# Kernel tuning notes

Hardware: AMD Instinct MI355X
Metric: run time of the kernel (lower is better)

The kernel has to match this reference:

```python
import jax, jax.numpy as jnp
import numpy as np

T, K = 2048, 6          # tokens, activated experts per token
DIM = 2048              # model dim
INTER = 1408            # moe intermediate dim
E = 16                  # routed experts (group_size, shared not fused)


def setup_inputs() -> dict:
    key = jax.random.key(0)
    k1, k2, k3, k4, k5, k6 = jax.random.split(key, 6)
    x = jax.random.normal(k1, (T, DIM), dtype=jnp.float32)
    weights = jax.random.uniform(k2, (T, K), dtype=jnp.float32)
    indices = jax.random.randint(k3, (T, K), 0, E, dtype=jnp.int64)
    s = 1.0 / np.sqrt(DIM)
    Wg = jax.random.normal(k4, (E, INTER, DIM), dtype=jnp.float32) * s
    Wu = jax.random.normal(k5, (E, INTER, DIM), dtype=jnp.float32) * s
    Wd = jax.random.normal(k6, (E, DIM, INTER), dtype=jnp.float32) * (1.0 / np.sqrt(INTER))
    return {"x": x, "weights": weights, "indices": indices,
            "Wg": Wg, "Wu": Wu, "Wd": Wd}


def reference(x, weights, indices, Wg, Wu, Wd):
    # per-token combine weight for each expert: [T, E]
    # gate_w[t, e] = sum_k weights[t, k] * (indices[t, k] == e)
    one_hot = jax.nn.one_hot(indices, E, dtype=x.dtype)        # [T, K, E]
    gate_w = jnp.einsum('tk,tke->te', weights, one_hot)        # [T, E]

    # SwiGLU expert FFN, dense over experts, combine folded pre-down-proj
    g = jnp.einsum('td,eid->tei', x, Wg)                       # [T, E, INTER]
    u = jnp.einsum('td,eid->tei', x, Wu)                       # [T, E, INTER]
    act = jax.nn.silu(g) * u                                   # [T, E, INTER]
    # y[t] = sum_e gate_w[t,e] * (act[t,e] @ Wd[e].T)
    y = jnp.einsum('tei,edi->td', act * gate_w[:, :, None], Wd)  # [T, DIM]
    return y
```

## Files before the change

### kernel.cpp

```cpp
#include <hip/hip_runtime.h>
#include <hip/hip_bf16.h>
#include <cstdint>

#define TT     2048
#define KSEL   6
#define DMODEL 2048
#define DINTER 1408
#define NE     16
#define PMAX   (TT * KSEL)

typedef short bf16x8 __attribute__((ext_vector_type(8)));
typedef float f32x4 __attribute__((ext_vector_type(4)));
typedef unsigned short u16;
typedef u16 u16x8 __attribute__((ext_vector_type(8)));

__device__ __forceinline__ u16 f2bf(float f) {
  union { float f; unsigned u; } v; v.f = f;
  return (u16)((v.u + 0x7FFFu + ((v.u >> 16) & 1u)) >> 16);
}

__device__ __forceinline__ void gl2lds16(const void* g, void* l) {
  __builtin_amdgcn_global_load_lds((const __attribute__((address_space(1))) void*)g,
                                   (__attribute__((address_space(3))) void*)l,
                                   16, 0, 0);
}

__global__ void k_gate(const float* __restrict__ w, const int* __restrict__ idx,
                       float* __restrict__ gate_w, int* __restrict__ counts) {
  int g = blockIdx.x * 256 + threadIdx.x;
  int t = g >> 4, e = g & 15;
  const int* ip = idx + t * KSEL;
  const float* wp = w + t * KSEL;
  float s = 0.f;
#pragma unroll
  for (int k = 0; k < KSEL; ++k) s += (ip[k] == e) ? wp[k] : 0.f;
  gate_w[g] = s;
  if (s != 0.f) atomicAdd(counts + e, 1);
}

__global__ void k_scan(const int* __restrict__ counts, int* __restrict__ offs) {
  if (threadIdx.x == 0 && blockIdx.x == 0) {
    int r = 0;
#pragma unroll
    for (int e = 0; e < NE; ++e) { offs[e] = r; r += counts[e]; }
    offs[NE] = r;
  }
}

__global__ void k_fill(const float* __restrict__ gate_w, const int* __restrict__ offs,
                       int* __restrict__ cursor, int* __restrict__ slot_tok,
                       float* __restrict__ slot_gate) {
  int g = blockIdx.x * 256 + threadIdx.x;
  int t = g >> 4, e = g & 15;
  float s = gate_w[g];
  if (s != 0.f) {
    int p = atomicAdd(cursor + e, 1);
    int sl = offs[e] + p;
    slot_tok[sl] = t;
    slot_gate[sl] = s;
  }
}

#define XV8   (TT * DMODEL / 8)
#define WV8   (NE * DINTER * DMODEL / 8)
__global__ void k_castall(const float* __restrict__ x,  u16* __restrict__ xb,
                          const float* __restrict__ wg, u16* __restrict__ wgb,
                          const float* __restrict__ wu, u16* __restrict__ wub,
                          const float* __restrict__ wd, u16* __restrict__ wdb) {
  const int total = XV8 + 3 * WV8;
  int stride = gridDim.x * 256;
  for (int i = blockIdx.x * 256 + threadIdx.x; i < total; i += stride) {
    const float* src; u16* dst; int j;
    if (i < XV8)                { src = x;  dst = xb;  j = i; }
    else if (i < XV8 + WV8)     { src = wg; dst = wgb; j = i - XV8; }
    else if (i < XV8 + 2 * WV8) { src = wu; dst = wub; j = i - XV8 - WV8; }
    else                        { src = wd; dst = wdb; j = i - XV8 - 2 * WV8; }
    const float4* p = (const float4*)src + (size_t)j * 2;
    float4 v0 = p[0], v1 = p[1];
    u16x8 o;
    o[0] = f2bf(v0.x); o[1] = f2bf(v0.y); o[2] = f2bf(v0.z); o[3] = f2bf(v0.w);
    o[4] = f2bf(v1.x); o[5] = f2bf(v1.y); o[6] = f2bf(v1.z); o[7] = f2bf(v1.w);
    *(u16x8*)(dst + (size_t)j * 8) = o;
  }
}


__global__ __launch_bounds__(256, 2) void k_gemm1(
    const u16* __restrict__ xb, const u16* __restrict__ wgb, const u16* __restrict__ wub,
    const int* __restrict__ slot_tok, const float* __restrict__ slot_gate,
    const int* __restrict__ offs, const int* __restrict__ counts,
    u16* __restrict__ act) {
  int b = blockIdx.x;
  int w = (b & 7) * 352 + (b >> 3);
  int mt = w & 15, rest = w >> 4;
  int it = rest % 11, e = rest / 11;

  int mcount = counts[e];
  if (mt * 128 >= mcount) return;
  int mrem = mcount - mt * 128; if (mrem > 128) mrem = 128;
  int slotBase = offs[e] + mt * 128;
  int iBase = it * 128;

  __shared__ u16 sA[128 * 64];
  __shared__ u16 sG[128 * 64];
  __shared__ u16 sU[128 * 64];
  __shared__ int tokLds[128];
  __shared__ float gateLds[128];

  int tid = threadIdx.x;
  if (tid < 128) {
    int rl = tid < mrem ? tid : 0;
    tokLds[tid] = slot_tok[slotBase + rl];
    gateLds[tid] = (tid < mrem) ? slot_gate[slotBase + rl] : 0.f;
  }
  __syncthreads();

  int wv = tid >> 6, lane = tid & 63;
  const u16 *aSrc[4], *gSrc[4], *uSrc[4];
  u16 *aDst[4], *gDst[4], *uDst[4];
  const u16* gBase = wgb + ((size_t)e * DINTER + iBase) * DMODEL;
  const u16* uBase = wub + ((size_t)e * DINTER + iBase) * DMODEL;
  int r8 = lane >> 3;
  int colOff = ((lane & 7) ^ r8) * 8;
#pragma unroll
  for (int i2 = 0; i2 < 4; ++i2) {
    int chunk = wv * 4 + i2;
    int row = chunk * 8 + r8;
    aSrc[i2] = xb + (size_t)tokLds[row] * DMODEL + colOff;
    gSrc[i2] = gBase + (size_t)row * DMODEL + colOff;
    uSrc[i2] = uBase + (size_t)row * DMODEL + colOff;
    aDst[i2] = sA + chunk * 512;
    gDst[i2] = sG + chunk * 512;
    uDst[i2] = sU + chunk * 512;
  }

  f32x4 accg[4][4] = {};
  f32x4 accu[4][4] = {};
  int fr = lane & 15, fq = lane >> 4;
  int wr = (wv >> 1) * 64, wc = (wv & 1) * 64;

  for (int kb = 0; kb < DMODEL / 64; ++kb) {
    int kOff = kb * 64;
    __syncthreads();
#pragma unroll
    for (int i2 = 0; i2 < 4; ++i2) {
      gl2lds16(aSrc[i2] + kOff, aDst[i2]);
      gl2lds16(gSrc[i2] + kOff, gDst[i2]);
      gl2lds16(uSrc[i2] + kOff, uDst[i2]);
    }
    __syncthreads();
#pragma unroll
    for (int kf = 0; kf < 2; ++kf) {
      bf16x8 af[4], bg[4], bu[4];
#pragma unroll
      for (int mf = 0; mf < 4; ++mf) {
        int row = wr + mf * 16 + fr;
        int cu = ((kf * 4 + fq) ^ (row & 7)) * 8;
        af[mf] = *(const bf16x8*)&sA[row * 64 + cu];
      }
#pragma unroll
      for (int nf = 0; nf < 4; ++nf) {
        int row = wc + nf * 16 + fr;
        int cu = ((kf * 4 + fq) ^ (row & 7)) * 8;
        bg[nf] = *(const bf16x8*)&sG[row * 64 + cu];
        bu[nf] = *(const bf16x8*)&sU[row * 64 + cu];
      }
#pragma unroll
      for (int mf = 0; mf < 4; ++mf)
#pragma unroll
        for (int nf = 0; nf < 4; ++nf) {
          accg[mf][nf] = __builtin_amdgcn_mfma_f32_16x16x32_bf16(af[mf], bg[nf], accg[mf][nf], 0, 0, 0);
          accu[mf][nf] = __builtin_amdgcn_mfma_f32_16x16x32_bf16(af[mf], bu[nf], accu[mf][nf], 0, 0, 0);
        }
    }
  }
#pragma unroll
  for (int mf = 0; mf < 4; ++mf)
#pragma unroll
    for (int nf = 0; nf < 4; ++nf)
#pragma unroll
      for (int r = 0; r < 4; ++r) {
        int row = wr + mf * 16 + fq * 4 + r;
        if (row < mrem) {
          float g = accg[mf][nf][r], u = accu[mf][nf][r];
          float a = g / (1.f + __expf(-g)) * u * gateLds[row];
          act[(size_t)(slotBase + row) * DINTER + iBase + wc + nf * 16 + fr] = f2bf(a);
        }
      }
}

__global__ __launch_bounds__(256, 3) void k_gemm2(
    const u16* __restrict__ act, const u16* __restrict__ wdb,
    const int* __restrict__ slot_tok, const int* __restrict__ offs,
    const int* __restrict__ counts, float* __restrict__ y) {
  int b = blockIdx.x;
  int w = (b & 7) * 512 + (b >> 3);
  int mt = w & 15, rest = w >> 4;
  int dt = rest & 15, e = rest >> 4;

  int mcount = counts[e];
  if (mt * 128 >= mcount) return;
  int mrem = mcount - mt * 128; if (mrem > 128) mrem = 128;
  int slotBase = offs[e] + mt * 128;
  int dBase = dt * 128;

  __shared__ u16 sA[128 * 64];
  __shared__ u16 sB[128 * 64];
  __shared__ int tokLds[128];

  int tid = threadIdx.x;
  if (tid < 128) tokLds[tid] = slot_tok[slotBase + (tid < mrem ? tid : 0)];
  __syncthreads();

  int wv = tid >> 6, lane = tid & 63;
  const u16 *aSrc[4], *bSrc[4];
  u16 *aDst[4], *bDst[4];
  const u16* bBase = wdb + ((size_t)e * DMODEL + dBase) * DINTER;
  int r8 = lane >> 3;
  int colOff = ((lane & 7) ^ r8) * 8;
#pragma unroll
  for (int i2 = 0; i2 < 4; ++i2) {
    int chunk = wv * 4 + i2;
    int row = chunk * 8 + r8;
    aSrc[i2] = act + (size_t)(slotBase + row) * DINTER + colOff;
    bSrc[i2] = bBase + (size_t)row * DINTER + colOff;
    aDst[i2] = sA + chunk * 512;
    bDst[i2] = sB + chunk * 512;
  }

  f32x4 acc[4][4] = {};
  int fr = lane & 15, fq = lane >> 4;
  int wr = (wv >> 1) * 64, wc = (wv & 1) * 64;

  for (int kb = 0; kb < DINTER / 64; ++kb) {
    int kOff = kb * 64;
    __syncthreads();
#pragma unroll
    for (int i2 = 0; i2 < 4; ++i2) {
      gl2lds16(aSrc[i2] + kOff, aDst[i2]);
      gl2lds16(bSrc[i2] + kOff, bDst[i2]);
    }
    __syncthreads();
#pragma unroll
    for (int kf = 0; kf < 2; ++kf) {
      bf16x8 af[4], bb[4];
#pragma unroll
      for (int mf = 0; mf < 4; ++mf) {
        int row = wr + mf * 16 + fr;
        int cu = ((kf * 4 + fq) ^ (row & 7)) * 8;
        af[mf] = *(const bf16x8*)&sA[row * 64 + cu];
      }
#pragma unroll
      for (int nf = 0; nf < 4; ++nf) {
        int row = wc + nf * 16 + fr;
        int cu = ((kf * 4 + fq) ^ (row & 7)) * 8;
        bb[nf] = *(const bf16x8*)&sB[row * 64 + cu];
      }
#pragma unroll
      for (int mf = 0; mf < 4; ++mf)
#pragma unroll
        for (int nf = 0; nf < 4; ++nf)
          acc[mf][nf] = __builtin_amdgcn_mfma_f32_16x16x32_bf16(af[mf], bb[nf], acc[mf][nf], 0, 0, 0);
    }
  }
#pragma unroll
  for (int mf = 0; mf < 4; ++mf)
#pragma unroll
    for (int nf = 0; nf < 4; ++nf)
#pragma unroll
      for (int r = 0; r < 4; ++r) {
        int row = wr + mf * 16 + fq * 4 + r;
        if (row < mrem) {
          int t = tokLds[row];
          atomicAdd(y + (size_t)t * DMODEL + dBase + wc + nf * 16 + fr, acc[mf][nf][r]);
        }
      }
}

extern "C" void kernel_launch(void* const* d_in, const int* in_sizes, int n_in,
                              void* d_out, int out_size, void* d_ws, size_t ws_size,
                              hipStream_t stream) {
  const float* x       = (const float*)d_in[0];
  const float* weights = (const float*)d_in[1];
  const int*   indices = (const int*)d_in[2];
  const float* Wg      = (const float*)d_in[3];
  const float* Wu      = (const float*)d_in[4];
  const float* Wd      = (const float*)d_in[5];
  float* y = (float*)d_out;

  const size_t WELEM = (size_t)NE * DINTER * DMODEL;

  char* ws = (char*)d_ws;
  size_t o = 0;
  float* gate_w = (float*)(ws + o); o += (size_t)TT * NE * 4;
  size_t ctrlOff = o;
  int* counts = (int*)(ws + o);
  int* offs   = (int*)(ws + o + 64);
  int* cursor = (int*)(ws + o + 192);
  o += 256;
  int*   slot_tok  = (int*)(ws + o);   o += (size_t)PMAX * 4;
  float* slot_gate = (float*)(ws + o); o += (size_t)PMAX * 4;
  u16* xb  = (u16*)(ws + o); o += (size_t)TT * DMODEL * 2;
  u16* act = (u16*)(ws + o); o += (size_t)(PMAX + 128) * DINTER * 2;
  u16* wgb = (u16*)(ws + o); o += WELEM * 2;
  u16* wub = (u16*)(ws + o); o += WELEM * 2;
  u16* wdb = (u16*)(ws + o); o += WELEM * 2;
  (void)ws_size; (void)in_sizes; (void)n_in;

  hipMemsetAsync(d_out, 0, (size_t)out_size * 4, stream);
  hipMemsetAsync(ws + ctrlOff, 0, 256, stream);

  k_gate<<<TT * NE / 256, 256, 0, stream>>>(weights, indices, gate_w, counts);
  k_scan<<<1, 64, 0, stream>>>(counts, offs);
  k_fill<<<TT * NE / 256, 256, 0, stream>>>(gate_w, offs, cursor, slot_tok, slot_gate);
  k_castall<<<2048, 256, 0, stream>>>(x, xb, Wg, wgb, Wu, wub, Wd, wdb);
  k_gemm1<<<2816, 256, 0, stream>>>(xb, wgb, wub, slot_tok, slot_gate, offs, counts, act);
  k_gemm2<<<4096, 256, 0, stream>>>(act, wdb, slot_tok, offs, counts, y);
}
```

Measured before the change: 590.4 us.

## Enlarge down-projection tile to 256 rows to reuse Wd tile twice

```diff
diff --git a/kernel.cpp b/kernel.cpp
--- a/kernel.cpp
+++ b/kernel.cpp
@@ -189,32 +189,38 @@
       }
 }
 
-__global__ __launch_bounds__(256, 3) void k_gemm2(
+__global__ __launch_bounds__(256, 2) void k_gemm2(
     const u16* __restrict__ act, const u16* __restrict__ wdb,
     const int* __restrict__ slot_tok, const int* __restrict__ offs,
     const int* __restrict__ counts, float* __restrict__ y) {
   int b = blockIdx.x;
-  int w = (b & 7) * 512 + (b >> 3);
-  int mt = w & 15, rest = w >> 4;
+  int w = (b & 7) * 256 + (b >> 3);
+  int mtp = w & 7, rest = w >> 3;
   int dt = rest & 15, e = rest >> 4;
 
   int mcount = counts[e];
-  if (mt * 128 >= mcount) return;
-  int mrem = mcount - mt * 128; if (mrem > 128) mrem = 128;
-  int slotBase = offs[e] + mt * 128;
+  if (mtp * 256 >= mcount) return;
+  int rem = mcount - mtp * 256;
+  int mrem0 = rem > 128 ? 128 : rem;
+  int mrem1 = rem > 128 ? (rem - 128 > 128 ? 128 : rem - 128) : 0;
+  int slotBase = offs[e] + mtp * 256;
   int dBase = dt * 128;
 
-  __shared__ u16 sA[128 * 64];
+  __shared__ u16 sA0[128 * 64];
+  __shared__ u16 sA1[128 * 64];
   __shared__ u16 sB[128 * 64];
-  __shared__ int tokLds[128];
+  __shared__ int tokLds[256];
 
   int tid = threadIdx.x;
-  if (tid < 128) tokLds[tid] = slot_tok[slotBase + (tid < mrem ? tid : 0)];
+  if (tid < 256) {
+    int lim = rem > 256 ? 256 : rem;
+    tokLds[tid] = slot_tok[slotBase + (tid < lim ? tid : 0)];
+  }
   __syncthreads();
 
   int wv = tid >> 6, lane = tid & 63;
-  const u16 *aSrc[4], *bSrc[4];
-  u16 *aDst[4], *bDst[4];
+  const u16 *a0Src[4], *a1Src[4], *bSrc[4];
+  u16 *a0Dst[4], *a1Dst[4], *bDst[4];
   const u16* bBase = wdb + ((size_t)e * DMODEL + dBase) * DINTER;
   int r8 = lane >> 3;
   int colOff = ((lane & 7) ^ r8) * 8;
@@ -222,13 +228,16 @@
   for (int i2 = 0; i2 < 4; ++i2) {
     int chunk = wv * 4 + i2;
     int row = chunk * 8 + r8;
-    aSrc[i2] = act + (size_t)(slotBase + row) * DINTER + colOff;
-    bSrc[i2] = bBase + (size_t)row * DINTER + colOff;
-    aDst[i2] = sA + chunk * 512;
-    bDst[i2] = sB + chunk * 512;
-  }
-
-  f32x4 acc[4][4] = {};
+    a0Src[i2] = act + (size_t)(slotBase + row) * DINTER + colOff;
+    a1Src[i2] = act + (size_t)(slotBase + 128 + row) * DINTER + colOff;
+    bSrc[i2]  = bBase + (size_t)row * DINTER + colOff;
+    a0Dst[i2] = sA0 + chunk * 512;
+    a1Dst[i2] = sA1 + chunk * 512;
+    bDst[i2]  = sB + chunk * 512;
+  }
+
+  f32x4 acc0[4][4] = {};
+  f32x4 acc1[4][4] = {};
   int fr = lane & 15, fq = lane >> 4;
   int wr = (wv >> 1) * 64, wc = (wv & 1) * 64;
 
@@ -237,18 +246,20 @@
     __syncthreads();
 #pragma unroll
     for (int i2 = 0; i2 < 4; ++i2) {
-      gl2lds16(aSrc[i2] + kOff, aDst[i2]);
+      gl2lds16(a0Src[i2] + kOff, a0Dst[i2]);
+      gl2lds16(a1Src[i2] + kOff, a1Dst[i2]);
       gl2lds16(bSrc[i2] + kOff, bDst[i2]);
     }
     __syncthreads();
 #pragma unroll
     for (int kf = 0; kf < 2; ++kf) {
-      bf16x8 af[4], bb[4];
+      bf16x8 a0f[4], a1f[4], bb[4];
 #pragma unroll
       for (int mf = 0; mf < 4; ++mf) {
         int row = wr + mf * 16 + fr;
         int cu = ((kf * 4 + fq) ^ (row & 7)) * 8;
-        af[mf] = *(const bf16x8*)&sA[row * 64 + cu];
+        a0f[mf] = *(const bf16x8*)&sA0[row * 64 + cu];
+        a1f[mf] = *(const bf16x8*)&sA1[row * 64 + cu];
       }
 #pragma unroll
       for (int nf = 0; nf < 4; ++nf) {
@@ -259,8 +270,10 @@
 #pragma unroll
       for (int mf = 0; mf < 4; ++mf)
 #pragma unroll
-        for (int nf = 0; nf < 4; ++nf)
-          acc[mf][nf] = __builtin_amdgcn_mfma_f32_16x16x32_bf16(af[mf], bb[nf], acc[mf][nf], 0, 0, 0);
+        for (int nf = 0; nf < 4; ++nf) {
+          acc0[mf][nf] = __builtin_amdgcn_mfma_f32_16x16x32_bf16(a0f[mf], bb[nf], acc0[mf][nf], 0, 0, 0);
+          acc1[mf][nf] = __builtin_amdgcn_mfma_f32_16x16x32_bf16(a1f[mf], bb[nf], acc1[mf][nf], 0, 0, 0);
+        }
     }
   }
 #pragma unroll
@@ -270,9 +283,12 @@
 #pragma unroll
       for (int r = 0; r < 4; ++r) {
         int row = wr + mf * 16 + fq * 4 + r;
-        if (row < mrem) {
-          int t = tokLds[row];
-          atomicAdd(y + (size_t)t * DMODEL + dBase + wc + nf * 16 + fr, acc[mf][nf][r]);
+        int col = dBase + wc + nf * 16 + fr;
+        if (row < mrem0) {
+          atomicAdd(y + (size_t)tokLds[row] * DMODEL + col, acc0[mf][nf][r]);
+        }
+        if (row < mrem1) {
+          atomicAdd(y + (size_t)tokLds[128 + row] * DMODEL + col, acc1[mf][nf][r]);
         }
       }
 }
@@ -301,7 +317,7 @@
   int*   slot_tok  = (int*)(ws + o);   o += (size_t)PMAX * 4;
   float* slot_gate = (float*)(ws + o); o += (size_t)PMAX * 4;
   u16* xb  = (u16*)(ws + o); o += (size_t)TT * DMODEL * 2;
-  u16* act = (u16*)(ws + o); o += (size_t)(PMAX + 128) * DINTER * 2;
+  u16* act = (u16*)(ws + o); o += (size_t)(PMAX + 256) * DINTER * 2;
   u16* wgb = (u16*)(ws + o); o += WELEM * 2;
   u16* wub = (u16*)(ws + o); o += WELEM * 2;
   u16* wdb = (u16*)(ws + o); o += WELEM * 2;
@@ -315,5 +331,5 @@
   k_fill<<<TT * NE / 256, 256, 0, stream>>>(gate_w, offs, cursor, slot_tok, slot_gate);
   k_castall<<<2048, 256, 0, stream>>>(x, xb, Wg, wgb, Wu, wub, Wd, wdb);
   k_gemm1<<<2816, 256, 0, stream>>>(xb, wgb, wub, slot_tok, slot_gate, offs, counts, act);
-  k_gemm2<<<4096, 256, 0, stream>>>(act, wdb, slot_tok, offs, counts, y);
-}
+  k_gemm2<<<2048, 256, 0, stream>>>(act, wdb, slot_tok, offs, counts, y);
+}
```

Measured after the change: 601.8 us. Within noise of the previous version (+1.9%).

## Replace down-proj atomic scatter with per-slot bf16 outputs and a gather-combine kernel

Applied to the files above, without the earlier changes.

```diff
diff --git a/kernel.cpp b/kernel.cpp
--- a/kernel.cpp
+++ b/kernel.cpp
@@ -17,6 +17,9 @@
 __device__ __forceinline__ u16 f2bf(float f) {
   union { float f; unsigned u; } v; v.f = f;
   return (u16)((v.u + 0x7FFFu + ((v.u >> 16) & 1u)) >> 16);
+}
+__device__ __forceinline__ float bf2f(u16 h) {
+  union { unsigned u; float f; } v; v.u = (unsigned)h << 16; return v.f;
 }
 
 __device__ __forceinline__ void gl2lds16(const void* g, void* l) {
@@ -49,7 +52,8 @@
 
 __global__ void k_fill(const float* __restrict__ gate_w, const int* __restrict__ offs,
                        int* __restrict__ cursor, int* __restrict__ slot_tok,
-                       float* __restrict__ slot_gate) {
+                       float* __restrict__ slot_gate, int* __restrict__ tcnt,
+                       int* __restrict__ tok_slots) {
   int g = blockIdx.x * 256 + threadIdx.x;
   int t = g >> 4, e = g & 15;
   float s = gate_w[g];
@@ -58,6 +62,8 @@
     int sl = offs[e] + p;
     slot_tok[sl] = t;
     slot_gate[sl] = s;
+    int q = atomicAdd(tcnt + t, 1);
+    tok_slots[t * KSEL + q] = sl;
   }
 }
 
@@ -192,7 +198,8 @@
 __global__ __launch_bounds__(256, 3) void k_gemm2(
     const u16* __restrict__ act, const u16* __restrict__ wdb,
     const int* __restrict__ slot_tok, const int* __restrict__ offs,
-    const int* __restrict__ counts, float* __restrict__ y) {
+    const int* __restrict__ counts, float* __restrict__ y,
+    u16* __restrict__ outb) {
   int b = blockIdx.x;
   int w = (b & 7) * 512 + (b >> 3);
   int mt = w & 15, rest = w >> 4;
@@ -271,10 +278,32 @@
       for (int r = 0; r < 4; ++r) {
         int row = wr + mf * 16 + fq * 4 + r;
         if (row < mrem) {
-          int t = tokLds[row];
-          atomicAdd(y + (size_t)t * DMODEL + dBase + wc + nf * 16 + fr, acc[mf][nf][r]);
+          int col = dBase + wc + nf * 16 + fr;
+          if (outb) {
+            outb[(size_t)(slotBase + row) * DMODEL + col] = f2bf(acc[mf][nf][r]);
+          } else {
+            atomicAdd(y + (size_t)tokLds[row] * DMODEL + col, acc[mf][nf][r]);
+          }
         }
       }
+}
+
+__global__ void k_combine(const u16* __restrict__ outb, const int* __restrict__ tok_slots,
+                          const int* __restrict__ tcnt, float* __restrict__ y) {
+  int idx = blockIdx.x * 256 + threadIdx.x;
+  int t = idx >> 8;
+  int d0 = (idx & 255) * 8;
+  int n = tcnt[t];
+  float s[8] = {};
+  for (int j = 0; j < n; ++j) {
+    int sl = tok_slots[t * KSEL + j];
+    u16x8 v = *(const u16x8*)(outb + (size_t)sl * DMODEL + d0);
+#pragma unroll
+    for (int q = 0; q < 8; ++q) s[q] += bf2f(v[q]);
+  }
+  float4* yp = (float4*)(y + (size_t)t * DMODEL + d0);
+  yp[0] = make_float4(s[0], s[1], s[2], s[3]);
+  yp[1] = make_float4(s[4], s[5], s[6], s[7]);
 }
 
 extern "C" void kernel_launch(void* const* d_in, const int* in_sizes, int n_in,
@@ -297,7 +326,10 @@
   int* counts = (int*)(ws + o);
   int* offs   = (int*)(ws + o + 64);
   int* cursor = (int*)(ws + o + 192);
-  o += 256;
+  int* tcnt   = (int*)(ws + o + 256);
+  int* tok_slots = (int*)(ws + o + 256 + TT * 4);
+  size_t ctrlZero = 256 + TT * 4;
+  o += 256 + TT * 4 + (size_t)TT * KSEL * 4;
   int*   slot_tok  = (int*)(ws + o);   o += (size_t)PMAX * 4;
   float* slot_gate = (float*)(ws + o); o += (size_t)PMAX * 4;
   u16* xb  = (u16*)(ws + o); o += (size_t)TT * DMODEL * 2;
@@ -305,15 +337,23 @@
   u16* wgb = (u16*)(ws + o); o += WELEM * 2;
   u16* wub = (u16*)(ws + o); o += WELEM * 2;
   u16* wdb = (u16*)(ws + o); o += WELEM * 2;
-  (void)ws_size; (void)in_sizes; (void)n_in;
+  u16* outb = (u16*)(ws + o);
+  size_t oEnd = o + (size_t)PMAX * DMODEL * 2;
+  bool useCombine = (ws_size >= oEnd);
+  (void)in_sizes; (void)n_in;
 
   hipMemsetAsync(d_out, 0, (size_t)out_size * 4, stream);
-  hipMemsetAsync(ws + ctrlOff, 0, 256, stream);
+  hipMemsetAsync(ws + ctrlOff, 0, ctrlZero, stream);
 
   k_gate<<<TT * NE / 256, 256, 0, stream>>>(weights, indices, gate_w, counts);
   k_scan<<<1, 64, 0, stream>>>(counts, offs);
-  k_fill<<<TT * NE / 256, 256, 0, stream>>>(gate_w, offs, cursor, slot_tok, slot_gate);
+  k_fill<<<TT * NE / 256, 256, 0, stream>>>(gate_w, offs, cursor, slot_tok, slot_gate,
+                                            tcnt, tok_slots);
   k_castall<<<2048, 256, 0, stream>>>(x, xb, Wg, wgb, Wu, wub, Wd, wdb);
   k_gemm1<<<2816, 256, 0, stream>>>(xb, wgb, wub, slot_tok, slot_gate, offs, counts, act);
-  k_gemm2<<<4096, 256, 0, stream>>>(act, wdb, slot_tok, offs, counts, y);
-}
+  k_gemm2<<<4096, 256, 0, stream>>>(act, wdb, slot_tok, offs, counts, y,
+                                    useCombine ? outb : (u16*)nullptr);
+  if (useCombine) {
+    k_combine<<<TT * DMODEL / 8 / 256, 256, 0, stream>>>(outb, tok_slots, tcnt, y);
+  }
+}
```

Result: no change. 581.2 us (-1.6%).
